# Performance work log

Hardware: AMD Instinct MI355X
Metric: run time of the kernel (lower is better)

The kernel has to match this reference:

```python
import jax, jax.numpy as jnp
import numpy as np

# Circuit structure constants (must match input_specs)
V, K, C = 128, 32, 256   # vars, input nodes per var, categories (V*K == N)
L, N, F = 4, 4096, 16    # layer pairs, sum nodes per layer, sum fan-in
E, B = 8192, 512         # product elements per layer, batch size
EPS = 1e-6


def setup_inputs() -> dict:
    key = jax.random.key(0)
    ks = jax.random.split(key, 6)
    return {
        "inputs": jax.random.randint(ks[0], (B, V), 0, C),
        "prod_child_ids": jax.random.randint(ks[1], (L, E, 2), 0, N),
        "sum_child_ids": jax.random.randint(ks[2], (L, N, F), 0, E),
        "input_params": jax.random.uniform(ks[3], (V, K, C), dtype=jnp.float32),
        "sum_params": jax.random.uniform(ks[4], (L, N, F), dtype=jnp.float32),
        "root_params": jax.random.uniform(ks[5], (N,), dtype=jnp.float32),
    }


def _forward(inputs, prod_child_ids, sum_child_ids, input_params, sum_params, root_params):
    # --- input layer: categorical leaves -> node_mars [V*K, B] (log space) ---
    lw_in = jnp.log(input_params + EPS)
    lw_in = lw_in - jax.nn.logsumexp(lw_in, axis=-1, keepdims=True)  # normalized log-params
    x = inputs.T  # [V, B]
    nm = lw_in[jnp.arange(V)[:, None, None], jnp.arange(K)[None, :, None], x[:, None, :]]  # [V, K, B]
    nm = nm.reshape(V * K, B)  # node_mars for leaves, V*K == N

    # --- normalized sum-layer log-weights ---
    lw_sum = jnp.log(sum_params + EPS)
    lw_sum = lw_sum - jax.nn.logsumexp(lw_sum, axis=-1, keepdims=True)  # [L, N, F]

    # --- alternating prod / sum layer groups (fixed small L) ---
    for l in range(L):
        # product layer: element_mars[e] = sum of child node_mars (log space add)
        em = nm[prod_child_ids[l, :, 0]] + nm[prod_child_ids[l, :, 1]]  # [E, B]
        # sum layer: node_mars[n] = logsumexp_j(element_mars[child j] + log w[n, j])
        ch = em[sum_child_ids[l]]  # [N, F, B] irregular gather
        nm = jax.nn.logsumexp(ch + lw_sum[l][:, :, None], axis=1)  # [N, B]

    # --- root sum node -> log-likelihoods [B] ---
    lr = jnp.log(root_params + EPS)
    lr = lr - jax.nn.logsumexp(lr)
    return jax.nn.logsumexp(nm + lr[:, None], axis=0)  # [B]


def reference(inputs, prod_child_ids, sum_child_ids, input_params, sum_params, root_params):
    return _forward(inputs, prod_child_ids, sum_child_ids, input_params, sum_params, root_params)
```

## Files before the change

### kernel.cpp

```cpp
#include <hip/hip_runtime.h>
#include <hip/hip_fp16.h>
#include <math.h>

#define V_ 128
#define K_ 32
#define C_ 256
#define L_ 4
#define N_ 4096
#define F_ 16
#define E_ 8192
#define B_ 512
#define EPS_ 1e-6f

__device__ __forceinline__ __half2 u2h(unsigned u) {
    __half2 h; *reinterpret_cast<unsigned*>(&h) = u; return h;
}
__device__ __forceinline__ unsigned h2u(__half2 h) {
    return *reinterpret_cast<unsigned*>(&h);
}
__device__ __forceinline__ __half b2h(unsigned short u) {
    __half h; *reinterpret_cast<unsigned short*>(&h) = u; return h;
}
__device__ __forceinline__ unsigned short h2b(__half h) {
    return *reinterpret_cast<unsigned short*>(&h);
}
__device__ __forceinline__ __half2 hmax2(__half2 a, __half2 b) {
    float2 fa = __half22float2(a), fb = __half22float2(b);
    return __floats2half2_rn(fmaxf(fa.x, fb.x), fmaxf(fa.y, fb.y));
}

__global__ __launch_bounds__(256) void prep_kernel(const float* __restrict__ sp,
                                                   const int* __restrict__ prod,
                                                   const int* __restrict__ sc,
                                                   const float* __restrict__ ip,
                                                   const float* __restrict__ rp,
                                                   unsigned* __restrict__ PIW,
                                                   unsigned* __restrict__ PP,
                                                   float* __restrict__ inv_row,
                                                   float* __restrict__ lrpsum) {
    int blk = blockIdx.x;
    int tid = threadIdx.x;
    if (blk < 64) {
        int idx = blk * 256 + tid;
        int l   = idx >> 12;
        int n   = idx & (N_ - 1);
        const float4* row4 = (const float4*)(sp + (size_t)idx * F_);
        float v[F_];
        float s = 0.f;
#pragma unroll
        for (int q = 0; q < 4; q++) {
            float4 r = row4[q];
            v[4*q+0] = r.x + EPS_; v[4*q+1] = r.y + EPS_;
            v[4*q+2] = r.z + EPS_; v[4*q+3] = r.w + EPS_;
            s += v[4*q+0] + v[4*q+1] + v[4*q+2] + v[4*q+3];
        }
        float inv = 1.f / s;
        const int* scr = sc + (size_t)idx * F_;
        uint4* dst = (uint4*)PIW + ((size_t)l * 4) * N_ + n;
#pragma unroll
        for (int q = 0; q < 4; q++) {
            uint4 o;
            o.x = (unsigned)(unsigned short)(scr[4*q+0] << 2) |
                  ((unsigned)h2b(__float2half(v[4*q+0] * inv)) << 16);
            o.y = (unsigned)(unsigned short)(scr[4*q+1] << 2) |
                  ((unsigned)h2b(__float2half(v[4*q+1] * inv)) << 16);
            o.z = (unsigned)(unsigned short)(scr[4*q+2] << 2) |
                  ((unsigned)h2b(__float2half(v[4*q+2] * inv)) << 16);
            o.w = (unsigned)(unsigned short)(scr[4*q+3] << 2) |
                  ((unsigned)h2b(__float2half(v[4*q+3] * inv)) << 16);
            dst[(size_t)q * N_] = o;
        }
    } else if (blk < 192) {
        int idx = (blk - 64) * 256 + tid;
        int2 c  = ((const int2*)prod)[idx];
        PP[idx] = ((unsigned)c.x << 2) | ((unsigned)c.y << 18);
    } else if (blk < 192 + 1024) {
        int rblk = blk - 192;
        int n    = rblk * 4 + (tid >> 6);
        int lane = tid & 63;
        const float* row = ip + (size_t)n * C_;
        float t = 0.f;
#pragma unroll
        for (int i = 0; i < 4; i++) t += row[lane + 64 * i] + EPS_;
#pragma unroll
        for (int off = 32; off; off >>= 1) t += __shfl_down(t, off, 64);
        if (lane == 0) inv_row[n] = 1.f / t;
    } else {
        __shared__ float smem[4];
        float acc = 0.f;
        for (int i = tid; i < N_; i += 256) acc += rp[i] + EPS_;
#pragma unroll
        for (int off = 32; off; off >>= 1) acc += __shfl_down(acc, off, 64);
        if ((tid & 63) == 0) smem[tid >> 6] = acc;
        __syncthreads();
        if (tid == 0) lrpsum[0] = __logf(smem[0] + smem[1] + smem[2] + smem[3]);
    }
}


#define SSTEP(QQ, ACC) { unsigned q_ = (QQ); \
    (ACC) = __hfma2(u2h(*(const unsigned*)((const char*)em + (q_ & 0xfffcu))), \
                    u2h(__builtin_amdgcn_perm(q_, q_, 0x03020302u)), (ACC)); }

#define PSTEP(QQ, DST) { unsigned q_ = (QQ); \
    __half2 t0_ = __hmul2(u2h(*(const unsigned*)((const char*)nm + (q_ & 0xfffcu))), ha); \
    __half2 t1_ = __hmul2(u2h(*(const unsigned*)((const char*)nm + (q_ >> 16))), ha); \
    (DST) = h2u(__hmul2(t0_, t1_)); }

__global__ __launch_bounds__(1024) void mega_kernel(const float* __restrict__ ip,
                                                    const int* __restrict__ inputs,
                                                    const float* __restrict__ inv_row,
                                                    const float* __restrict__ rp,
                                                    const unsigned* __restrict__ PIW,
                                                    const unsigned* __restrict__ PP,
                                                    const float* __restrict__ lrpsum,
                                                    float* __restrict__ out) {
    __shared__ __align__(16) unsigned em[E_];
    __shared__ __align__(16) unsigned nm[N_];
    __shared__ unsigned redm[16];
    __shared__ float    redf[32];
    int tid  = threadIdx.x;
    int lane = tid & 63;
    int w    = tid >> 6;
    int b0   = blockIdx.x * 2, b1 = b0 + 1;

    float2 u[4];
    float mx0 = 0.f, mx1 = 0.f;
#pragma unroll
    for (int p = 0; p < 4; p++) {
        int n  = p * 1024 + tid;
        int v  = n >> 5;
        int x0 = inputs[b0 * V_ + v];
        int x1 = inputs[b1 * V_ + v];
        float invr = inv_row[n];
        u[p].x = (ip[(size_t)n * C_ + x0] + EPS_) * invr;
        u[p].y = (ip[(size_t)n * C_ + x1] + EPS_) * invr;
        mx0 = fmaxf(mx0, u[p].x);
        mx1 = fmaxf(mx1, u[p].y);
    }
#pragma unroll
    for (int off = 32; off; off >>= 1) {
        mx0 = fmaxf(mx0, __shfl_down(mx0, off, 64));
        mx1 = fmaxf(mx1, __shfl_down(mx1, off, 64));
    }
    if (lane == 0) { redf[w] = mx0; redf[16 + w] = mx1; }
    __syncthreads();
    float m0 = redf[0], m1 = redf[16];
#pragma unroll
    for (int i = 1; i < 16; i++) { m0 = fmaxf(m0, redf[i]); m1 = fmaxf(m1, redf[16 + i]); }
    float inv0 = 1.f / m0, inv1 = 1.f / m1;
    float sg0 = __logf(m0), sg1 = __logf(m1);
#pragma unroll
    for (int p = 0; p < 4; p++)
        nm[p * 1024 + tid] = h2u(__floats2half2_rn(u[p].x * inv0, u[p].y * inv1));
    __syncthreads();

    __half2 ha  = __floats2half2_rn(1.f, 1.f);
    float   af0 = 1.f, af1 = 1.f;

    for (int l = 0; l < L_ - 1; l++) {
        const uint4* pp4 = (const uint4*)(PP + (size_t)l * E_);
#pragma unroll
        for (int p = 0; p < 2; p++) {
            uint4 c = pp4[p * 1024 + tid];
            uint4 o;
            PSTEP(c.x, o.x); PSTEP(c.y, o.y); PSTEP(c.z, o.z); PSTEP(c.w, o.w);
            ((uint4*)em)[p * 1024 + tid] = o;
        }
        sg0 = 2.f * sg0 + 2.f * __logf(af0);
        sg1 = 2.f * sg1 + 2.f * __logf(af1);
        __syncthreads();

        const uint4* piw4 = (const uint4*)PIW + (size_t)l * 4 * N_;
        __half2 hm = u2h(0u);
#pragma unroll
        for (int p = 0; p < 4; p++) {
            int n = p * 1024 + tid;
            uint4 q0 = piw4[n];
            uint4 q1 = piw4[N_ + n];
            uint4 q2 = piw4[2 * N_ + n];
            uint4 q3 = piw4[3 * N_ + n];
            __half2 a0 = u2h(0u), a1 = u2h(0u);
            SSTEP(q0.x, a0) SSTEP(q0.y, a1) SSTEP(q0.z, a0) SSTEP(q0.w, a1)
            SSTEP(q1.x, a0) SSTEP(q1.y, a1) SSTEP(q1.z, a0) SSTEP(q1.w, a1)
            SSTEP(q2.x, a0) SSTEP(q2.y, a1) SSTEP(q2.z, a0) SSTEP(q2.w, a1)
            SSTEP(q3.x, a0) SSTEP(q3.y, a1) SSTEP(q3.z, a0) SSTEP(q3.w, a1)
            __half2 acc = __hadd2(a0, a1);
            nm[n] = h2u(acc);
            hm    = hmax2(hm, acc);
        }
#pragma unroll
        for (int off = 32; off; off >>= 1)
            hm = hmax2(hm, u2h(__shfl_down(h2u(hm), off, 64)));
        if (lane == 0) redm[w] = h2u(hm);
        __syncthreads();
        __half2 M = u2h(redm[0]);
#pragma unroll
        for (int i = 1; i < 16; i++) M = hmax2(M, u2h(redm[i]));
        float M0 = __half2float(__low2half(M)), M1 = __half2float(__high2half(M));
        ha  = __floats2half2_rn(fminf(1.f / M0, 60000.f), fminf(1.f / M1, 60000.f));
        af0 = __half2float(__low2half(ha));
        af1 = __half2float(__high2half(ha));
        sg0 -= 2.f * __logf(af0);
        sg1 -= 2.f * __logf(af1);
    }

    {
        const uint4* pp4 = (const uint4*)(PP + (size_t)(L_ - 1) * E_);
#pragma unroll
        for (int p = 0; p < 2; p++) {
            uint4 c = pp4[p * 1024 + tid];
            uint4 o;
            PSTEP(c.x, o.x); PSTEP(c.y, o.y); PSTEP(c.z, o.z); PSTEP(c.w, o.w);
            ((uint4*)em)[p * 1024 + tid] = o;
        }
        sg0 = 2.f * sg0 + 2.f * __logf(af0);
        sg1 = 2.f * sg1 + 2.f * __logf(af1);
        __syncthreads();

        const uint4* piw4 = (const uint4*)PIW + (size_t)(L_ - 1) * 4 * N_;
        float S0 = 0.f, S1 = 0.f;
#pragma unroll
        for (int p = 0; p < 4; p++) {
            int n = p * 1024 + tid;
            uint4 q0 = piw4[n];
            uint4 q1 = piw4[N_ + n];
            uint4 q2 = piw4[2 * N_ + n];
            uint4 q3 = piw4[3 * N_ + n];
            __half2 a0 = u2h(0u), a1 = u2h(0u);
            SSTEP(q0.x, a0) SSTEP(q0.y, a1) SSTEP(q0.z, a0) SSTEP(q0.w, a1)
            SSTEP(q1.x, a0) SSTEP(q1.y, a1) SSTEP(q1.z, a0) SSTEP(q1.w, a1)
            SSTEP(q2.x, a0) SSTEP(q2.y, a1) SSTEP(q2.z, a0) SSTEP(q2.w, a1)
            SSTEP(q3.x, a0) SSTEP(q3.y, a1) SSTEP(q3.z, a0) SSTEP(q3.w, a1)
            float2 vv = __half22float2(__hadd2(a0, a1));
            float  r  = rp[n] + EPS_;
            S0 += r * vv.x;
            S1 += r * vv.y;
        }
#pragma unroll
        for (int off = 32; off; off >>= 1) {
            S0 += __shfl_down(S0, off, 64);
            S1 += __shfl_down(S1, off, 64);
        }
        if (lane == 0) { redf[w] = S0; redf[16 + w] = S1; }
        __syncthreads();
        if (tid == 0) {
            float s0 = 0.f, s1 = 0.f;
#pragma unroll
            for (int i = 0; i < 16; i++) { s0 += redf[i]; s1 += redf[16 + i]; }
            float lr = lrpsum[0];
            out[b0] = __logf(s0) + sg0 - lr;
            out[b1] = __logf(s1) + sg1 - lr;
        }
    }
}

extern "C" void kernel_launch(void* const* d_in, const int* in_sizes, int n_in,
                              void* d_out, int out_size, void* d_ws, size_t ws_size,
                              hipStream_t stream) {
    const int*   inputs = (const int*)d_in[0];
    const int*   prod   = (const int*)d_in[1];
    const int*   sc     = (const int*)d_in[2];
    const float* ip     = (const float*)d_in[3];
    const float* sp     = (const float*)d_in[4];
    const float* rp     = (const float*)d_in[5];
    float* out = (float*)d_out;

    unsigned* PIW     = (unsigned*)d_ws;
    unsigned* PP      = PIW + (size_t)L_ * N_ * F_;
    float*    inv_row = (float*)(PP + (size_t)L_ * E_);
    float*    lrpsum  = inv_row + N_;

    prep_kernel<<<64 + 128 + 1024 + 1, 256, 0, stream>>>(sp, prod, sc, ip, rp,
                                                         PIW, PP, inv_row, lrpsum);
    mega_kernel<<<B_ / 2, 1024, 0, stream>>>(ip, inputs, inv_row, rp,
                                             PIW, PP, lrpsum, out);
}
```

Measured before the change: 105.5 us.

## Software-prefetch layer params across barriers and use LDS-only barriers

Prefetches the next sum-node index/weight quads and the next layer's product child ids into registers one iteration ahead, so global loads overlap with LDS gather compute and with barriers. Replaces __syncthreads with a barrier that waits only on LDS counters, so in-flight global prefetches are not drained at each sync. Also uses the packed f16 max instruction for hmax2 and preloads the root params. This raises register pressure, and the LDS-only barrier relies on the global loads not being needed before the sync.

After: 104.0 us. Within noise of the previous version (-1.4%).

```diff
diff --git a/kernel.cpp b/kernel.cpp
--- a/kernel.cpp
+++ b/kernel.cpp
@@ -25,8 +25,13 @@
     return *reinterpret_cast<unsigned short*>(&h);
 }
 __device__ __forceinline__ __half2 hmax2(__half2 a, __half2 b) {
-    float2 fa = __half22float2(a), fb = __half22float2(b);
-    return __floats2half2_rn(fmaxf(fa.x, fb.x), fmaxf(fa.y, fb.y));
+    unsigned r, ua = h2u(a), ub = h2u(b);
+    asm("v_pk_max_f16 %0, %1, %2" : "=v"(r) : "v"(ua), "v"(ub));
+    return u2h(r);
+}
+__device__ __forceinline__ void barrier_lds_only() {
+    asm volatile("s_waitcnt lgkmcnt(0)" ::: "memory");
+    __builtin_amdgcn_s_barrier();
 }
 
 __global__ __launch_bounds__(256) void prep_kernel(const float* __restrict__ sp,
@@ -153,38 +158,49 @@
 #pragma unroll
     for (int p = 0; p < 4; p++)
         nm[p * 1024 + tid] = h2u(__floats2half2_rn(u[p].x * inv0, u[p].y * inv1));
-    __syncthreads();
+
+    const uint4* pp0 = (const uint4*)PP;
+    uint4 cA = pp0[tid], cB = pp0[1024 + tid];
+    barrier_lds_only();
 
     __half2 ha  = __floats2half2_rn(1.f, 1.f);
     float   af0 = 1.f, af1 = 1.f;
 
     for (int l = 0; l < L_ - 1; l++) {
-        const uint4* pp4 = (const uint4*)(PP + (size_t)l * E_);
-#pragma unroll
-        for (int p = 0; p < 2; p++) {
-            uint4 c = pp4[p * 1024 + tid];
+        const uint4* piw4 = (const uint4*)PIW + (size_t)l * 4 * N_;
+        uint4 q0 = piw4[tid];
+        uint4 q1 = piw4[N_ + tid];
+        uint4 q2 = piw4[2 * N_ + tid];
+        uint4 q3 = piw4[3 * N_ + tid];
+        {
             uint4 o;
-            PSTEP(c.x, o.x); PSTEP(c.y, o.y); PSTEP(c.z, o.z); PSTEP(c.w, o.w);
-            ((uint4*)em)[p * 1024 + tid] = o;
+            PSTEP(cA.x, o.x); PSTEP(cA.y, o.y); PSTEP(cA.z, o.z); PSTEP(cA.w, o.w);
+            ((uint4*)em)[tid] = o;
+            PSTEP(cB.x, o.x); PSTEP(cB.y, o.y); PSTEP(cB.z, o.z); PSTEP(cB.w, o.w);
+            ((uint4*)em)[1024 + tid] = o;
         }
         sg0 = 2.f * sg0 + 2.f * __logf(af0);
         sg1 = 2.f * sg1 + 2.f * __logf(af1);
-        __syncthreads();
-
-        const uint4* piw4 = (const uint4*)PIW + (size_t)l * 4 * N_;
+        barrier_lds_only();
+
+        const uint4* ppn = (const uint4*)PP + (size_t)(l + 1) * (E_ / 4);
         __half2 hm = u2h(0u);
 #pragma unroll
         for (int p = 0; p < 4; p++) {
             int n = p * 1024 + tid;
-            uint4 q0 = piw4[n];
-            uint4 q1 = piw4[N_ + n];
-            uint4 q2 = piw4[2 * N_ + n];
-            uint4 q3 = piw4[3 * N_ + n];
+            uint4 r0 = q0, r1 = q1, r2 = q2, r3 = q3;
+            if (p < 3) {
+                int nn = n + 1024;
+                q0 = piw4[nn]; q1 = piw4[N_ + nn];
+                q2 = piw4[2 * N_ + nn]; q3 = piw4[3 * N_ + nn];
+            } else {
+                cA = ppn[tid]; cB = ppn[1024 + tid];
+            }
             __half2 a0 = u2h(0u), a1 = u2h(0u);
-            SSTEP(q0.x, a0) SSTEP(q0.y, a1) SSTEP(q0.z, a0) SSTEP(q0.w, a1)
-            SSTEP(q1.x, a0) SSTEP(q1.y, a1) SSTEP(q1.z, a0) SSTEP(q1.w, a1)
-            SSTEP(q2.x, a0) SSTEP(q2.y, a1) SSTEP(q2.z, a0) SSTEP(q2.w, a1)
-            SSTEP(q3.x, a0) SSTEP(q3.y, a1) SSTEP(q3.z, a0) SSTEP(q3.w, a1)
+            SSTEP(r0.x, a0) SSTEP(r0.y, a1) SSTEP(r0.z, a0) SSTEP(r0.w, a1)
+            SSTEP(r1.x, a0) SSTEP(r1.y, a1) SSTEP(r1.z, a0) SSTEP(r1.w, a1)
+            SSTEP(r2.x, a0) SSTEP(r2.y, a1) SSTEP(r2.z, a0) SSTEP(r2.w, a1)
+            SSTEP(r3.x, a0) SSTEP(r3.y, a1) SSTEP(r3.z, a0) SSTEP(r3.w, a1)
             __half2 acc = __hadd2(a0, a1);
             nm[n] = h2u(acc);
             hm    = hmax2(hm, acc);
@@ -193,7 +209,7 @@
         for (int off = 32; off; off >>= 1)
             hm = hmax2(hm, u2h(__shfl_down(h2u(hm), off, 64)));
         if (lane == 0) redm[w] = h2u(hm);
-        __syncthreads();
+        barrier_lds_only();
         __half2 M = u2h(redm[0]);
 #pragma unroll
         for (int i = 1; i < 16; i++) M = hmax2(M, u2h(redm[i]));
@@ -206,34 +222,41 @@
     }
 
     {
-        const uint4* pp4 = (const uint4*)(PP + (size_t)(L_ - 1) * E_);
-#pragma unroll
-        for (int p = 0; p < 2; p++) {
-            uint4 c = pp4[p * 1024 + tid];
+        const uint4* piw4 = (const uint4*)PIW + (size_t)(L_ - 1) * 4 * N_;
+        uint4 q0 = piw4[tid];
+        uint4 q1 = piw4[N_ + tid];
+        uint4 q2 = piw4[2 * N_ + tid];
+        uint4 q3 = piw4[3 * N_ + tid];
+        float rv0 = rp[tid], rv1 = rp[1024 + tid],
+              rv2 = rp[2048 + tid], rv3 = rp[3072 + tid];
+        {
             uint4 o;
-            PSTEP(c.x, o.x); PSTEP(c.y, o.y); PSTEP(c.z, o.z); PSTEP(c.w, o.w);
-            ((uint4*)em)[p * 1024 + tid] = o;
+            PSTEP(cA.x, o.x); PSTEP(cA.y, o.y); PSTEP(cA.z, o.z); PSTEP(cA.w, o.w);
+            ((uint4*)em)[tid] = o;
+            PSTEP(cB.x, o.x); PSTEP(cB.y, o.y); PSTEP(cB.z, o.z); PSTEP(cB.w, o.w);
+            ((uint4*)em)[1024 + tid] = o;
         }
         sg0 = 2.f * sg0 + 2.f * __logf(af0);
         sg1 = 2.f * sg1 + 2.f * __logf(af1);
-        __syncthreads();
-
-        const uint4* piw4 = (const uint4*)PIW + (size_t)(L_ - 1) * 4 * N_;
+        barrier_lds_only();
+
         float S0 = 0.f, S1 = 0.f;
 #pragma unroll
         for (int p = 0; p < 4; p++) {
             int n = p * 1024 + tid;
-            uint4 q0 = piw4[n];
-            uint4 q1 = piw4[N_ + n];
-            uint4 q2 = piw4[2 * N_ + n];
-            uint4 q3 = piw4[3 * N_ + n];
+            uint4 r0 = q0, r1 = q1, r2 = q2, r3 = q3;
+            if (p < 3) {
+                int nn = n + 1024;
+                q0 = piw4[nn]; q1 = piw4[N_ + nn];
+                q2 = piw4[2 * N_ + nn]; q3 = piw4[3 * N_ + nn];
+            }
             __half2 a0 = u2h(0u), a1 = u2h(0u);
-            SSTEP(q0.x, a0) SSTEP(q0.y, a1) SSTEP(q0.z, a0) SSTEP(q0.w, a1)
-            SSTEP(q1.x, a0) SSTEP(q1.y, a1) SSTEP(q1.z, a0) SSTEP(q1.w, a1)
-            SSTEP(q2.x, a0) SSTEP(q2.y, a1) SSTEP(q2.z, a0) SSTEP(q2.w, a1)
-            SSTEP(q3.x, a0) SSTEP(q3.y, a1) SSTEP(q3.z, a0) SSTEP(q3.w, a1)
+            SSTEP(r0.x, a0) SSTEP(r0.y, a1) SSTEP(r0.z, a0) SSTEP(r0.w, a1)
+            SSTEP(r1.x, a0) SSTEP(r1.y, a1) SSTEP(r1.z, a0) SSTEP(r1.w, a1)
+            SSTEP(r2.x, a0) SSTEP(r2.y, a1) SSTEP(r2.z, a0) SSTEP(r2.w, a1)
+            SSTEP(r3.x, a0) SSTEP(r3.y, a1) SSTEP(r3.z, a0) SSTEP(r3.w, a1)
             float2 vv = __half22float2(__hadd2(a0, a1));
-            float  r  = rp[n] + EPS_;
+            float  r  = (p == 0 ? rv0 : p == 1 ? rv1 : p == 2 ? rv2 : rv3) + EPS_;
             S0 += r * vv.x;
             S1 += r * vv.y;
         }
```
